# Optimization experiments

Hardware: AMD Instinct MI355X
Metric: run time of the kernel (lower is better)

## Reference

```python
import jax, jax.numpy as jnp
from jax import lax
import numpy as np

B, H, W = 16, 512, 512
OPENING_R, EROSION_R, DILATION_R = 5, 2, 1
MIN_SIZE, AREA_THRESHOLD = 2000, 300
INF = np.int32(2 ** 30)


def _disk(r):
    # skimage.morphology.disk: x^2 + y^2 <= r^2 on a (2r+1)^2 grid
    y, x = np.mgrid[-r:r + 1, -r:r + 1]
    return jnp.asarray((x * x + y * y <= r * r).astype(np.float32))


D_OPEN, D_ERODE, D_DILATE = _disk(OPENING_R), _disk(EROSION_R), _disk(DILATION_R)


def _conv2(x, k):
    return lax.conv_general_dilated(x[None, None], k[None, None], (1, 1), 'VALID')[0, 0]


def _erode(fg, se):
    # skimage binary_erosion uses border_value=True (image border does not erode)
    r = se.shape[0] // 2
    x = jnp.pad(fg.astype(jnp.float32), r, constant_values=1.0)
    return _conv2(x, se) >= se.sum() - 0.5


def _dilate(fg, se):
    # skimage binary_dilation uses border_value=False
    r = se.shape[0] // 2
    x = jnp.pad(fg.astype(jnp.float32), r, constant_values=0.0)
    return _conv2(x, se) > 0.5


def _seg_cummin(v, reset, axis, reverse):
    # segmented cumulative-min: scan resets wherever `reset` is True (background)
    def comb(a, b):
        av, af = a
        bv, bf = b
        return jnp.where(bf, bv, jnp.minimum(av, bv)), af | bf

    vv, _ = lax.associative_scan(comb, (v, reset), axis=axis, reverse=reverse)
    return vv


def _label(fg):
    # 4-connectivity connected-component labeling via min-label propagation.
    # Each fg pixel starts with its raveled index; alternating row/col segmented
    # cummin sweeps run under while_loop until a fixed point (root id per comp).
    h, w = fg.shape
    idx = jnp.arange(h * w, dtype=jnp.int32).reshape(h, w)
    lab0 = jnp.where(fg, idx, INF)
    bg = ~fg

    def sweep(l):
        for axis in (1, 0):
            for rev in (False, True):
                l = jnp.where(fg, _seg_cummin(l, bg, axis, rev), INF)
        return l

    def body(c):
        l, _ = c
        nl = sweep(l)
        return nl, jnp.array_equal(nl, l)

    lab, _ = lax.while_loop(lambda c: ~c[1], body, (lab0, jnp.array(False)))
    seg = jnp.where(fg, lab, 0).ravel()
    sizes = jax.ops.segment_sum(fg.astype(jnp.int32).ravel(), seg, num_segments=h * w)
    ncomp = jnp.sum(sizes > 0)
    return lab, sizes, ncomp


def _remove_small_objects(fg, min_size, guard):
    lab, sizes, ncomp = _label(fg)
    px = sizes[jnp.where(fg, lab, 0)]  # component size at every fg pixel
    kept = fg & (px >= min_size)
    # original only removes small objects when label(...).max() > 1
    return jnp.where(ncomp > 1, kept, fg) if guard else kept


def _pipeline(mask):
    fg = mask > 0
    fg = _remove_small_objects(fg, MIN_SIZE, True)
    # remove_small_holes == ~remove_small_objects(~fg, area_threshold + 1)
    fg = ~_remove_small_objects(~fg, AREA_THRESHOLD + 1, False)
    fg = _erode(fg, D_ERODE)
    fg = _dilate(_erode(fg, D_OPEN), D_OPEN)  # binary_opening
    fg = _remove_small_objects(fg, MIN_SIZE, True)
    fg = _dilate(fg, D_DILATE)
    return fg.astype(jnp.float32)  # original casts to int; float32 kept for vjp parity


def setup_inputs() -> dict:
    key = jax.random.key(0)
    # blobby binary masks: threshold bilinearly-upsampled low-res noise so that
    # realistic large connected components (> min_size px) exist
    low = jax.random.uniform(key, (B, H // 16, W // 16), dtype=jnp.float32)
    blob = jax.image.resize(low, (B, H, W), method='bilinear')
    return {'inputs': (blob > 0.5).astype(jnp.float32)}


def reference(inputs):
    return jax.vmap(_pipeline)(inputs)
```

## Files before the change

kernel.cpp:

```cpp
#include <hip/hip_runtime.h>
#include <stdint.h>

#define BATCH 16
#define H 512
#define W 512
#define HW (H * W)
#define NTOT (BATCH * HW)
#define NWORDS (NTOT / 64)

#define SROWS 16
#define SWORDS 128
#define SPIX 8192
#define NSTRIPS (NWORDS / SWORDS)
#define NBOUND (BATCH * 248)

#define FLAG_STRIDE 16
#define SPIN_LIMIT (1 << 20)

__device__ __forceinline__ int ald(const int* p) {
    return __hip_atomic_load((int*)p, __ATOMIC_RELAXED, __HIP_MEMORY_SCOPE_AGENT);
}
__device__ __forceinline__ void ast(int* p, int v) {
    __hip_atomic_store(p, v, __ATOMIC_RELAXED, __HIP_MEMORY_SCOPE_AGENT);
}
__device__ __forceinline__ uint64_t ald64(const uint64_t* p) {
    return __hip_atomic_load((uint64_t*)p, __ATOMIC_RELAXED, __HIP_MEMORY_SCOPE_AGENT);
}
__device__ __forceinline__ void ast64(uint64_t* p, uint64_t v) {
    __hip_atomic_store(p, v, __ATOMIC_RELAXED, __HIP_MEMORY_SCOPE_AGENT);
}

__device__ __forceinline__ int find_root_c(int* L, int x) {
    int r = x, p = ald(&L[r]);
    while (p != r) { r = p; p = ald(&L[r]); }
    if (ald(&L[x]) != r) atomicMin(&L[x], r);
    return r;
}

__device__ void merge_uf(int* L, int a, int b) {
    while (true) {
        a = find_root_c(L, a);
        b = find_root_c(L, b);
        if (a == b) return;
        int lo = a < b ? a : b;
        int hi = a < b ? b : a;
        int old = atomicMin(&L[hi], lo);
        if (old == hi) return;
        a = lo; b = old;
    }
}

__device__ __forceinline__ int find_root_lds(int* P, int x) {
    int r = x, p = P[r];
    while (p != r) { r = p; p = P[r]; }
    return r;
}

__device__ void merge_lds(int* P, int a, int b) {
    while (true) {
        a = find_root_lds(P, a);
        b = find_root_lds(P, b);
        if (a == b) return;
        int lo = a < b ? a : b;
        int hi = a < b ? b : a;
        int old = atomicMin(&P[hi], lo);
        if (old == hi) return;
        a = lo; b = old;
    }
}

__device__ __forceinline__ int start_of(uint64_t m, int i, int cv, int base) {
    uint64_t below = i ? ((~m) & ((1ull << i) - 1)) : 0ull;
    if (below == 0) return (cv >= 0) ? cv : base;
    int hz = 63 - __builtin_clzll(below);
    return base + hz + 1;
}

__device__ uint64_t keep_word(const uint64_t* __restrict__ bits,
                              const int* __restrict__ carry, const int* __restrict__ L,
                              const int* __restrict__ sizes, const int* __restrict__ ncomp,
                              int minsz, int gw) {
    uint64_t m = ald64(&bits[gw]);
    uint64_t res = m;
    if (m && ald(&ncomp[gw >> 12]) > 1) {
        int cv = ald(&carry[gw]);
        int base = gw << 6;
        while (m) {
            int s = __builtin_ctzll(m);
            uint64_t rest = m >> s;
            uint64_t nr = ~rest;
            int len = nr ? __builtin_ctzll(nr) : (64 - s);
            uint64_t piece = ((len >= 64) ? ~0ull : ((1ull << len) - 1)) << s;
            int start = (s == 0 && cv >= 0) ? cv : (base + s);
            if (ald(&sizes[ald(&L[start])]) < minsz) res &= ~piece;
            m &= ~piece;
        }
    }
    return res;
}

__device__ uint64_t fill_word(const uint64_t* __restrict__ bits,
                              const int* __restrict__ carry, const int* __restrict__ L,
                              const int* __restrict__ sizes, int minsz, int gw) {
    uint64_t fg = ald64(&bits[gw]);
    uint64_t bg = ~fg;
    uint64_t res = fg;
    int cv = ald(&carry[gw]);
    int base = gw << 6;
    while (bg) {
        int s = __builtin_ctzll(bg);
        uint64_t rest = bg >> s;
        uint64_t nr = ~rest;
        int len = nr ? __builtin_ctzll(nr) : (64 - s);
        uint64_t piece = ((len >= 64) ? ~0ull : ((1ull << len) - 1)) << s;
        int start = (s == 0 && cv >= 0) ? cv : (base + s);
        if (ald(&sizes[ald(&L[start])]) < minsz) res |= piece;
        bg &= ~piece;
    }
    return res;
}

template <int R, bool ERODE>
__device__ uint64_t morph_word_lds(const uint64_t* buf, int lrow, int w, int gyTop) {
    const uint64_t BORDER = ERODE ? ~0ull : 0ull;
    uint64_t res = ERODE ? ~0ull : 0ull;
#pragma unroll
    for (int dy = -R; dy <= R; ++dy) {
        int lr = lrow + dy;
        int gy = gyTop + lr;
        if (gy < 0 || gy >= H) continue;
        int v = R * R - dy * dy;
        int kx = 0;
        while ((kx + 1) * (kx + 1) <= v) ++kx;
        uint64_t cur = buf[lr * 8 + w];
        uint64_t prv = (w > 0) ? buf[lr * 8 + w - 1] : BORDER;
        uint64_t nxt = (w < 7) ? buf[lr * 8 + w + 1] : BORDER;
        uint64_t acc = cur;
#pragma unroll
        for (int dx = 1; dx <= kx; ++dx) {
            uint64_t right = (cur >> dx) | (nxt << (64 - dx));
            uint64_t left  = (cur << dx) | (prv >> (64 - dx));
            if (ERODE) acc &= right & left;
            else       acc |= right | left;
        }
        if (ERODE) res &= acc;
        else       res |= acc;
    }
    return res;
}

__device__ void strip_ccl_body(uint64_t m, uint64_t* sw, int* scarry, int* par,
                               int blk, int t,
                               int* __restrict__ carry, int* __restrict__ L,
                               int* __restrict__ sizes, int* __restrict__ ncomp) {
    if (t < SWORDS) sw[t] = m;
    __syncthreads();

    if (t < SROWS) {
        int cv = -1;
        for (int i = 0; i < 8; ++i) {
            int lw = t * 8 + i;
            scarry[lw] = cv;
            uint64_t w = sw[lw];
            if (w >> 63) {
                uint64_t z = ~w;
                if (z == 0) { if (cv < 0) cv = lw << 6; }
                else { int hz = 63 - __builtin_clzll(z); cv = (lw << 6) + hz + 1; }
            } else cv = -1;
        }
    }
    __syncthreads();

    int lbase = t << 6;
    int cv = -1;
    uint64_t starts = 0ull;
    if (t < SWORDS) {
        cv = scarry[t];
        ast(&carry[blk * SWORDS + t], (cv >= 0) ? (blk * SPIX + cv) : -1);
        starts = m & ~((m << 1) | ((cv >= 0) ? 1ull : 0ull));
        uint64_t ss = starts;
        while (ss) {
            int s = __builtin_ctzll(ss);
            par[lbase + s] = lbase + s;
            ss &= ss - 1;
        }
    }
    __syncthreads();

    if (t >= 8 && t < SWORDS && m) {
        uint64_t up = sw[t - 8];
        uint64_t cand = m & up;
        if (cand) {
            uint64_t curprev = (t & 7) ? sw[t - 1] : 0ull;
            uint64_t upprev  = (t & 7) ? sw[t - 9] : 0ull;
            uint64_t curl = (m << 1) | (curprev >> 63);
            uint64_t upl  = (up << 1) | (upprev >> 63);
            cand &= ~(curl & upl);
            int cvu = scarry[t - 8];
            while (cand) {
                int i = __builtin_ctzll(cand);
                int sP = start_of(m, i, cv, lbase);
                int sQ = start_of(up, i, cvu, lbase - 512);
                merge_lds(par, sP, sQ);
                cand &= cand - 1;
            }
        }
    }
    __syncthreads();

    if (t < SWORDS) {
        int gpix = blk * SPIX;
        uint64_t ss = starts;
        while (ss) {
            int s = __builtin_ctzll(ss);
            int ls = lbase + s;
            int r = find_root_lds(par, ls);
            ast(&L[gpix + ls], gpix + r);
            if (r == ls) ast(&sizes[gpix + ls], 0);
            ss &= ss - 1;
        }
    }
    if (t == 0 && (blk & 31) == 0) ast(&ncomp[blk >> 5], 0);
}

__device__ void merge_bound_item(const uint64_t* __restrict__ bits, uint64_t inv64,
                                 const int* __restrict__ carry, int* __restrict__ L,
                                 int gw, int w) {
    uint64_t cur = ald64(&bits[gw]) ^ inv64;
    uint64_t up  = ald64(&bits[gw - 8]) ^ inv64;
    uint64_t cand = cur & up;
    if (!cand) return;
    uint64_t curprev = w ? (ald64(&bits[gw - 1]) ^ inv64) : 0ull;
    uint64_t upprev  = w ? (ald64(&bits[gw - 9]) ^ inv64) : 0ull;
    uint64_t curl = (cur << 1) | (curprev >> 63);
    uint64_t upl  = (up << 1)  | (upprev >> 63);
    cand &= ~(curl & upl);
    if (!cand) return;
    int cvc = ald(&carry[gw]), cvu = ald(&carry[gw - 8]);
    int base = gw << 6;
    while (cand) {
        int i = __builtin_ctzll(cand);
        int sP = start_of(cur, i, cvc, base);
        int sQ = start_of(up, i, cvu, base - W);
        merge_uf(L, sP, sQ);
        cand &= cand - 1;
    }
}

__device__ void flatten_block(const uint64_t* __restrict__ bits, uint64_t inv64,
                              const int* __restrict__ carry, int* __restrict__ L,
                              int* __restrict__ sizes, int* __restrict__ ncomp,
                              int blk, int t, int* hk, int* hv) {
    if (t < 128) { hk[t] = -1; hv[t] = 0; }
    __syncthreads();
    if (t < SWORDS) {
        int gw = blk * SWORDS + t;
        uint64_t m = ald64(&bits[gw]) ^ inv64;
        if (m) {
            int cv = ald(&carry[gw]);
            int base = gw << 6;
            while (m) {
                int s = __builtin_ctzll(m);
                uint64_t rest = m >> s;
                uint64_t nr = ~rest;
                int len = nr ? __builtin_ctzll(nr) : (64 - s);
                uint64_t piece = ((len >= 64) ? ~0ull : ((1ull << len) - 1)) << s;
                bool initial = !(s == 0 && cv >= 0);
                int start = initial ? (base + s) : cv;
                int r = find_root_c(L, start);
                if (initial && r == start) atomicAdd(&ncomp[gw >> 12], 1);
                int cnt = __popcll(piece);
                uint32_t h = ((uint32_t)r * 2654435761u) >> 25;
                bool done = false;
                for (int tt = 0; tt < 16; ++tt) {
                    int slot = (h + tt) & 127;
                    int k = hk[slot];
                    if (k == -1) k = atomicCAS(&hk[slot], -1, r);
                    if (k == -1 || k == r) { atomicAdd(&hv[slot], cnt); done = true; break; }
                }
                if (!done) atomicAdd(&sizes[r], cnt);
                m &= ~piece;
            }
        }
    }
    __syncthreads();
    if (t < 128 && hk[t] != -1) atomicAdd(&sizes[hk[t]], hv[t]);
}

__device__ void keep_dilate_seg(const uint64_t* __restrict__ bits,
                                const int* __restrict__ carry, const int* __restrict__ L,
                                const int* __restrict__ sizes, const int* __restrict__ ncomp,
                                float* __restrict__ out,
                                int img, int y0, int t, uint64_t* kb, uint64_t* db) {
    if (t < 80) {
        int lr = t >> 3;
        int w = t & 7;
        int gy = y0 - 1 + lr;
        uint64_t v = 0;
        if (gy >= 0 && gy < H)
            v = keep_word(bits, carry, L, sizes, ncomp, 2000, img * 4096 + gy * 8 + w);
        kb[t] = v;
    }
    __syncthreads();
    if (t < 64) {
        int r = t >> 3, w = t & 7;
        uint64_t cur = kb[(r + 1) * 8 + w];
        uint64_t up  = kb[r * 8 + w];
        uint64_t dn  = kb[(r + 2) * 8 + w];
        uint64_t prv = w ? kb[(r + 1) * 8 + w - 1] : 0ull;
        uint64_t nxt = (w < 7) ? kb[(r + 1) * 8 + w + 1] : 0ull;
        db[t] = cur | up | dn | (cur << 1) | (prv >> 63) | (cur >> 1) | (nxt << 63);
    }
    __syncthreads();

    int q0 = t * 16;
    uint64_t wd = db[q0 >> 6];
    int sh = q0 & 63;
    float4* o = (float4*)(out + (size_t)img * HW + (size_t)y0 * W + q0);
#pragma unroll
    for (int k = 0; k < 4; ++k) {
        uint32_t nib = (uint32_t)(wd >> (sh + k * 4)) & 0xFu;
        float4 f;
        f.x = (nib & 1u) ? 1.0f : 0.0f;
        f.y = (nib & 2u) ? 1.0f : 0.0f;
        f.z = (nib & 4u) ? 1.0f : 0.0f;
        f.w = (nib & 8u) ? 1.0f : 0.0f;
        o[k] = f;
    }
}

__device__ __forceinline__ void gbar(int* flags, int phase) {
    int* go = flags + NSTRIPS * FLAG_STRIDE;
    __syncthreads();
    if (threadIdx.x == 0) {
        asm volatile("s_waitcnt vmcnt(0)" ::: "memory");
        ast(&flags[blockIdx.x * FLAG_STRIDE], phase);
    }
    if (blockIdx.x == 0) {
        int spins = 0;
        while (ald(&flags[threadIdx.x * FLAG_STRIDE]) < phase && ++spins < SPIN_LIMIT)
            __builtin_amdgcn_s_sleep(1);
        while (ald(&flags[(threadIdx.x + 256) * FLAG_STRIDE]) < phase && ++spins < SPIN_LIMIT)
            __builtin_amdgcn_s_sleep(1);
        __syncthreads();
        if (threadIdx.x == 0) ast(go, phase);
    }
    if (threadIdx.x == 0) {
        int spins = 0;
        while (ald(go) < phase && ++spins < SPIN_LIMIT)
            __builtin_amdgcn_s_sleep(1);
    }
    __syncthreads();
}

__global__ __launch_bounds__(256, 2) void k_mega(
        const float4* __restrict__ in4, float* __restrict__ out,
        int* LA, int* sizesA, int* LB, int* sizesB,
        uint64_t* bits1, uint64_t* bits2, uint64_t* bits3,
        int* carryA, int* carryB, int* ncompA, int* ncompB, int* flags) {
    __shared__ uint64_t sw[SWORDS];
    __shared__ int scarry[SWORDS];
    __shared__ union US {
        int par[SPIX];
        struct { uint64_t A[320]; uint64_t B[320]; } mo;
        struct { int hk[128]; int hv[128]; } ha;
        struct { uint64_t kb[80]; uint64_t db[64]; } kd;
    } U;
    int blk = blockIdx.x;
    int t = threadIdx.x;

#pragma unroll
    for (int it = 0; it < 8; ++it) {
        int q = blk * (SPIX / 4) + it * 256 + t;
        float4 v = in4[q];
        uint32_t nib = (v.x > 0.0f ? 1u : 0u) | (v.y > 0.0f ? 2u : 0u) |
                       (v.z > 0.0f ? 4u : 0u) | (v.w > 0.0f ? 8u : 0u);
        uint64_t val = (uint64_t)nib << (4 * (t & 15));
        val |= __shfl_xor(val, 1);
        val |= __shfl_xor(val, 2);
        val |= __shfl_xor(val, 4);
        val |= __shfl_xor(val, 8);
        if ((t & 15) == 0) ast64(&bits1[q >> 4], val);
    }
    __syncthreads();

    {
        uint64_t m = (t < SWORDS) ? ald64(&bits1[blk * SWORDS + t]) : 0ull;
        strip_ccl_body(m, sw, scarry, U.par, blk, t, carryA, LA, sizesA, ncompA);
    }
    gbar(flags, 1);

    if (t < 8) {
        int item = blk * 8 + t;
        if (item < NBOUND) {
            int img = item / 248;
            int r = item - img * 248;
            int gw = img * 4096 + ((r >> 3) + 1) * SROWS * 8 + (r & 7);
            merge_bound_item(bits1, 0ull, carryA, LA, gw, r & 7);
        }
    }
    gbar(flags, 2);

    flatten_block(bits1, 0ull, carryA, LA, sizesA, ncompA, blk, t, U.ha.hk, U.ha.hv);
    gbar(flags, 3);

    {
        uint64_t m = 0ull;
        if (t < SWORDS) {
            int gw = blk * SWORDS + t;
            uint64_t kw = keep_word(bits1, carryA, LA, sizesA, ncompA, 2000, gw);
            ast64(&bits2[gw], kw);
            m = ~kw;
        }
        strip_ccl_body(m, sw, scarry, U.par, blk, t, carryB, LB, sizesB, ncompB);
    }
    gbar(flags, 4);

    if (t < 8) {
        int item = blk * 8 + t;
        if (item < NBOUND) {
            int img = item / 248;
            int r = item - img * 248;
            int gw = img * 4096 + ((r >> 3) + 1) * SROWS * 8 + (r & 7);
            merge_bound_item(bits2, ~0ull, carryB, LB, gw, r & 7);
        }
    }
    gbar(flags, 5);

    flatten_block(bits2, ~0ull, carryB, LB, sizesB, ncompB, blk, t, U.ha.hk, U.ha.hv);
    gbar(flags, 6);

    {
        int img = blk >> 5, si = blk & 31;
        int gyTop = si * 16 - 12;
        for (int lw = t; lw < 320; lw += 256) {
            int gy = gyTop + (lw >> 3);
            int w = lw & 7;
            uint64_t v = 0;
            if (gy >= 0 && gy < H)
                v = fill_word(bits2, carryB, LB, sizesB, 301, img * 4096 + gy * 8 + w);
            U.mo.A[lw] = v;
        }
        __syncthreads();
        for (int lw = t; lw < 320; lw += 256) {
            int lr = lw >> 3;
            if (lr >= 2 && lr <= 37) U.mo.B[lw] = morph_word_lds<2, true>(U.mo.A, lr, lw & 7, gyTop);
        }
        __syncthreads();
        for (int lw = t; lw < 320; lw += 256) {
            int lr = lw >> 3;
            if (lr >= 7 && lr <= 32) U.mo.A[lw] = morph_word_lds<5, true>(U.mo.B, lr, lw & 7, gyTop);
        }
        __syncthreads();
        for (int lw = t; lw < 320; lw += 256) {
            int lr = lw >> 3;
            if (lr >= 12 && lr <= 27) U.mo.B[lw] = morph_word_lds<5, false>(U.mo.A, lr, lw & 7, gyTop);
        }
        __syncthreads();
        uint64_t m3 = 0ull;
        if (t < SWORDS) {
            m3 = U.mo.B[t + 96];
            ast64(&bits3[blk * SWORDS + t], m3);
        }
        strip_ccl_body(m3, sw, scarry, U.par, blk, t, carryA, LA, sizesA, ncompA);
    }
    gbar(flags, 7);

    if (t < 8) {
        int item = blk * 8 + t;
        if (item < NBOUND) {
            int img = item / 248;
            int r = item - img * 248;
            int gw = img * 4096 + ((r >> 3) + 1) * SROWS * 8 + (r & 7);
            merge_bound_item(bits3, 0ull, carryA, LA, gw, r & 7);
        }
    }
    gbar(flags, 8);

    flatten_block(bits3, 0ull, carryA, LA, sizesA, ncompA, blk, t, U.ha.hk, U.ha.hv);
    gbar(flags, 9);

    for (int k = 0; k < 2; ++k) {
        int seg = blk * 2 + k;
        int img = seg >> 6, s8 = seg & 63;
        keep_dilate_seg(bits3, carryA, LA, sizesA, ncompA, out,
                        img, s8 * 8, t, U.kd.kb, U.kd.db);
        __syncthreads();
    }
}

extern "C" void kernel_launch(void* const* d_in, const int* in_sizes, int n_in,
                              void* d_out, int out_size, void* d_ws, size_t ws_size,
                              hipStream_t stream) {
    const float* in = (const float*)d_in[0];
    float* out = (float*)d_out;

    uint8_t* ws = (uint8_t*)d_ws;
    int* LA      = (int*)ws;
    int* sizesA  = (int*)(ws + (size_t)NTOT * 4);
    int* LB      = (int*)(ws + (size_t)NTOT * 8);
    int* sizesB  = (int*)(ws + (size_t)NTOT * 12);
    uint64_t* bits1 = (uint64_t*)(ws + (size_t)NTOT * 16);
    uint64_t* bits2 = bits1 + NWORDS;
    uint64_t* bits3 = bits2 + NWORDS;
    int* carryA = (int*)(bits3 + NWORDS);
    int* carryB = carryA + NWORDS;
    int* ncompA = carryB + NWORDS;
    int* ncompB = ncompA + BATCH;
    int* flags  = ncompB + BATCH;

    hipMemsetAsync(flags, 0, (NSTRIPS * FLAG_STRIDE + FLAG_STRIDE) * sizeof(int),
                   stream);

    k_mega<<<NSTRIPS, 256, 0, stream>>>((const float4*)in, out,
                                        LA, sizesA, LB, sizesB,
                                        bits1, bits2, bits3,
                                        carryA, carryB, ncompA, ncompB, flags);
}
```

Baseline: 194.0 us.

## Replace grid-wide barrier with per-image barriers among each image's strip blocks

The global barrier, where block 0 gathers all 512 flags and then broadcasts a go flag, is replaced by a per-image barrier. Each of the 32 blocks of an image polls its peers' flags directly. Boundary-merge work items are remapped so each image's blocks handle only that image's boundaries, which keeps all dependencies within one image. This removes the central gather and broadcast round trip and lets images advance through phases independently. In exchange, more lanes poll flags, and the flags are no longer padded to separate cache lines, so polling may contend.

```diff
diff --git a/kernel.cpp b/kernel.cpp
--- a/kernel.cpp
+++ b/kernel.cpp
@@ -12,9 +12,9 @@
 #define SWORDS 128
 #define SPIX 8192
 #define NSTRIPS (NWORDS / SWORDS)
-#define NBOUND (BATCH * 248)
-
-#define FLAG_STRIDE 16
+#define IMG_STRIPS 32
+#define NBOUND_IMG 248
+
 #define SPIN_LIMIT (1 << 20)
 
 __device__ __forceinline__ int ald(const int* p) {
@@ -329,25 +329,16 @@
     }
 }
 
-__device__ __forceinline__ void gbar(int* flags, int phase) {
-    int* go = flags + NSTRIPS * FLAG_STRIDE;
+__device__ __forceinline__ void ibar(int* flags, int img, int si, int phase) {
+    int* base = flags + img * 32;
     __syncthreads();
     if (threadIdx.x == 0) {
         asm volatile("s_waitcnt vmcnt(0)" ::: "memory");
-        ast(&flags[blockIdx.x * FLAG_STRIDE], phase);
-    }
-    if (blockIdx.x == 0) {
+        ast(&base[si], phase);
+    }
+    if (threadIdx.x < 32) {
         int spins = 0;
-        while (ald(&flags[threadIdx.x * FLAG_STRIDE]) < phase && ++spins < SPIN_LIMIT)
-            __builtin_amdgcn_s_sleep(1);
-        while (ald(&flags[(threadIdx.x + 256) * FLAG_STRIDE]) < phase && ++spins < SPIN_LIMIT)
-            __builtin_amdgcn_s_sleep(1);
-        __syncthreads();
-        if (threadIdx.x == 0) ast(go, phase);
-    }
-    if (threadIdx.x == 0) {
-        int spins = 0;
-        while (ald(go) < phase && ++spins < SPIN_LIMIT)
+        while (ald(&base[threadIdx.x]) < phase && ++spins < SPIN_LIMIT)
             __builtin_amdgcn_s_sleep(1);
     }
     __syncthreads();
@@ -368,6 +359,7 @@
     } U;
     int blk = blockIdx.x;
     int t = threadIdx.x;
+    int img = blk >> 5, si = blk & 31;
 
 #pragma unroll
     for (int it = 0; it < 8; ++it) {
@@ -388,21 +380,19 @@
         uint64_t m = (t < SWORDS) ? ald64(&bits1[blk * SWORDS + t]) : 0ull;
         strip_ccl_body(m, sw, scarry, U.par, blk, t, carryA, LA, sizesA, ncompA);
     }
-    gbar(flags, 1);
+    ibar(flags, img, si, 1);
 
     if (t < 8) {
-        int item = blk * 8 + t;
-        if (item < NBOUND) {
-            int img = item / 248;
-            int r = item - img * 248;
-            int gw = img * 4096 + ((r >> 3) + 1) * SROWS * 8 + (r & 7);
-            merge_bound_item(bits1, 0ull, carryA, LA, gw, r & 7);
-        }
-    }
-    gbar(flags, 2);
+        int item = si * 8 + t;
+        if (item < NBOUND_IMG) {
+            int gw = img * 4096 + ((item >> 3) + 1) * SROWS * 8 + (item & 7);
+            merge_bound_item(bits1, 0ull, carryA, LA, gw, item & 7);
+        }
+    }
+    ibar(flags, img, si, 2);
 
     flatten_block(bits1, 0ull, carryA, LA, sizesA, ncompA, blk, t, U.ha.hk, U.ha.hv);
-    gbar(flags, 3);
+    ibar(flags, img, si, 3);
 
     {
         uint64_t m = 0ull;
@@ -414,24 +404,21 @@
         }
         strip_ccl_body(m, sw, scarry, U.par, blk, t, carryB, LB, sizesB, ncompB);
     }
-    gbar(flags, 4);
+    ibar(flags, img, si, 4);
 
     if (t < 8) {
-        int item = blk * 8 + t;
-        if (item < NBOUND) {
-            int img = item / 248;
-            int r = item - img * 248;
-            int gw = img * 4096 + ((r >> 3) + 1) * SROWS * 8 + (r & 7);
-            merge_bound_item(bits2, ~0ull, carryB, LB, gw, r & 7);
-        }
-    }
-    gbar(flags, 5);
+        int item = si * 8 + t;
+        if (item < NBOUND_IMG) {
+            int gw = img * 4096 + ((item >> 3) + 1) * SROWS * 8 + (item & 7);
+            merge_bound_item(bits2, ~0ull, carryB, LB, gw, item & 7);
+        }
+    }
+    ibar(flags, img, si, 5);
 
     flatten_block(bits2, ~0ull, carryB, LB, sizesB, ncompB, blk, t, U.ha.hk, U.ha.hv);
-    gbar(flags, 6);
+    ibar(flags, img, si, 6);
 
     {
-        int img = blk >> 5, si = blk & 31;
         int gyTop = si * 16 - 12;
         for (int lw = t; lw < 320; lw += 256) {
             int gy = gyTop + (lw >> 3);
@@ -464,25 +451,23 @@
         }
         strip_ccl_body(m3, sw, scarry, U.par, blk, t, carryA, LA, sizesA, ncompA);
     }
-    gbar(flags, 7);
+    ibar(flags, img, si, 7);
 
     if (t < 8) {
-        int item = blk * 8 + t;
-        if (item < NBOUND) {
-            int img = item / 248;
-            int r = item - img * 248;
-            int gw = img * 4096 + ((r >> 3) + 1) * SROWS * 8 + (r & 7);
-            merge_bound_item(bits3, 0ull, carryA, LA, gw, r & 7);
-        }
-    }
-    gbar(flags, 8);
+        int item = si * 8 + t;
+        if (item < NBOUND_IMG) {
+            int gw = img * 4096 + ((item >> 3) + 1) * SROWS * 8 + (item & 7);
+            merge_bound_item(bits3, 0ull, carryA, LA, gw, item & 7);
+        }
+    }
+    ibar(flags, img, si, 8);
 
     flatten_block(bits3, 0ull, carryA, LA, sizesA, ncompA, blk, t, U.ha.hk, U.ha.hv);
-    gbar(flags, 9);
+    ibar(flags, img, si, 9);
 
     for (int k = 0; k < 2; ++k) {
         int seg = blk * 2 + k;
-        int img = seg >> 6, s8 = seg & 63;
+        int s8 = seg & 63;
         keep_dilate_seg(bits3, carryA, LA, sizesA, ncompA, out,
                         img, s8 * 8, t, U.kd.kb, U.kd.db);
         __syncthreads();
@@ -509,8 +494,7 @@
     int* ncompB = ncompA + BATCH;
     int* flags  = ncompB + BATCH;
 
-    hipMemsetAsync(flags, 0, (NSTRIPS * FLAG_STRIDE + FLAG_STRIDE) * sizeof(int),
-                   stream);
+    hipMemsetAsync(flags, 0, BATCH * 32 * sizeof(int), stream);
 
     k_mega<<<NSTRIPS, 256, 0, stream>>>((const float4*)in, out,
                                         LA, sizesA, LB, sizesB,
```

Result: no change. 192.9 us (-0.6%).
